# Kernel optimization log

Measured on AMD Instinct MI355X. Metric: run time of the kernel, lower is better.

Reference implementation:

```python
import jax, jax.numpy as jnp
import numpy as np

N = 200000   # 10000 graphs x 20 nodes, stacked
E = 3200000  # avg degree 16
F_IN = 4
H = 32
BN_EPS = 1e-5


def setup_inputs() -> dict:
    key = jax.random.key(0)
    ks = jax.random.split(key, 16)
    s = 0.1
    return {
        "x": jax.random.normal(ks[0], (N, F_IN), jnp.float32),
        "edge_index": jax.random.randint(ks[1], (2, E), 0, N, jnp.int64),
        "edge_weight": jax.random.uniform(ks[2], (E,), jnp.float32),
        "gcn1_w": jax.random.normal(ks[3], (F_IN, H), jnp.float32) * s,
        "gcn1_b": jnp.zeros((H,), jnp.float32),
        "gcn2_w": jax.random.normal(ks[4], (H, H), jnp.float32) * s,
        "gcn2_b": jnp.zeros((H,), jnp.float32),
        "bn1_gamma": jnp.ones((H,), jnp.float32),
        "bn1_beta": jnp.zeros((H,), jnp.float32),
        "bn1_mean": jnp.zeros((H,), jnp.float32),
        "bn1_var": jnp.ones((H,), jnp.float32),
        "bn2_gamma": jnp.ones((H,), jnp.float32),
        "bn2_beta": jnp.zeros((H,), jnp.float32),
        "bn2_mean": jnp.zeros((H,), jnp.float32),
        "bn2_var": jnp.ones((H,), jnp.float32),
        "lstm1_wih": jax.random.normal(ks[5], (4 * H, 2 * H), jnp.float32) * s,
        "lstm1_whh": jax.random.normal(ks[6], (4 * H, H), jnp.float32) * s,
        "lstm1_bih": jax.random.normal(ks[7], (4 * H,), jnp.float32) * s,
        "lstm1_bhh": jax.random.normal(ks[8], (4 * H,), jnp.float32) * s,
        "lstm2_wih": jax.random.normal(ks[9], (4 * H, H), jnp.float32) * s,
        "lstm2_whh": jax.random.normal(ks[10], (4 * H, H), jnp.float32) * s,
        "lstm2_bih": jax.random.normal(ks[11], (4 * H,), jnp.float32) * s,
        "lstm2_bhh": jax.random.normal(ks[12], (4 * H,), jnp.float32) * s,
        "lin_w": jax.random.normal(ks[13], (1, 2 * H + F_IN), jnp.float32) * s,
        "lin_b": jnp.zeros((1,), jnp.float32),
    }


def _gcn_conv(x, src, dst, ew, W, b, n):
    # GCNConv: x @ W, add self-loops (weight 1), symmetric normalization, scatter-add at dst.
    xw = x @ W
    loop = jnp.arange(n)
    s = jnp.concatenate([src, loop])
    d = jnp.concatenate([dst, loop])
    w = jnp.concatenate([ew, jnp.ones((n,), ew.dtype)])
    deg = jax.ops.segment_sum(w, d, num_segments=n)
    dinv = jnp.where(deg > 0, jax.lax.rsqrt(deg), 0.0)
    norm = dinv[s] * w * dinv[d]  # [E+N]
    out = jax.ops.segment_sum(norm[:, None] * xw[s], d, num_segments=n)
    return out + b


def _bn_eval(x, gamma, beta, mean, var):
    return (x - mean) * jax.lax.rsqrt(var + BN_EPS) * gamma + beta


def _lstm_step(x, wih, bih, bhh):
    # single timestep, zero initial (h, c): recurrent W_hh term vanishes.
    gates = x @ wih.T + bih + bhh
    i, f, g, o = jnp.split(gates, 4, axis=1)  # torch gate order i,f,g,o
    c = jax.nn.sigmoid(i) * jnp.tanh(g)
    return jax.nn.sigmoid(o) * jnp.tanh(c)


def reference(x, edge_index, edge_weight, gcn1_w, gcn1_b, gcn2_w, gcn2_b,
              bn1_gamma, bn1_beta, bn1_mean, bn1_var,
              bn2_gamma, bn2_beta, bn2_mean, bn2_var,
              lstm1_wih, lstm1_whh, lstm1_bih, lstm1_bhh,
              lstm2_wih, lstm2_whh, lstm2_bih, lstm2_bhh,
              lin_w, lin_b):
    n = x.shape[0]
    src, dst = edge_index[0], edge_index[1]
    # MPNNLSTM (window=1, eval mode: dropout=identity, BN uses running stats)
    h1 = _bn_eval(jax.nn.relu(_gcn_conv(x, src, dst, edge_weight, gcn1_w, gcn1_b, n)),
                  bn1_gamma, bn1_beta, bn1_mean, bn1_var)
    h2 = _bn_eval(jax.nn.relu(_gcn_conv(h1, src, dst, edge_weight, gcn2_w, gcn2_b, n)),
                  bn2_gamma, bn2_beta, bn2_mean, bn2_var)
    skip = jnp.concatenate([h1, h2], axis=1)  # [N, 2H]
    H1 = _lstm_step(skip, lstm1_wih, lstm1_bih, lstm1_bhh)  # [N, H]
    H2 = _lstm_step(H1, lstm2_wih, lstm2_bih, lstm2_bhh)    # [N, H]
    h = jnp.concatenate([H1, H2, x], axis=1)  # [N, 2H + F_IN]
    # RecurrentGCN head: relu + linear -> [N, 1]
    return jax.nn.relu(h) @ lin_w.T + lin_b
```

## Files before the change

### kernel.cpp

```cpp
#include <hip/hip_runtime.h>
#include <hip/hip_fp16.h>
#include <math.h>

#define BN_EPS 1e-5f
#define HF 32
#define BS 256
#define KEDGE 4096
#define MAXNB 800
#define WQ14 16383.0f
#define WQ22 4194303.0f

typedef _Float16 half8 __attribute__((ext_vector_type(8)));
typedef float f32x4 __attribute__((ext_vector_type(4)));
typedef float f32x2 __attribute__((ext_vector_type(2)));

__device__ __forceinline__ float fsig(float x) {
    return __builtin_amdgcn_rcpf(1.0f + __expf(-x));
}
__device__ __forceinline__ float ftanh(float x) {
    return 1.0f - 2.0f * __builtin_amdgcn_rcpf(1.0f + __expf(2.0f * x));
}


__device__ __forceinline__ float e4m3_to_f32_sw(unsigned v) {
    unsigned s = v & 0x80u, E = (v >> 3) & 0xFu, m = v & 7u;
    float r = E ? ldexpf((float)(8 + m), (int)E - 10) : ldexpf((float)m, -9);
    return s ? -r : r;
}

__device__ __forceinline__ unsigned f32_to_e4m3_sw(float x) {
    float ax = fabsf(x);
    unsigned s = x < 0.0f ? 0x80u : 0u;
    if (!(ax > 0.0f)) return s;
    if (ax >= 448.0f) return s | 0x7Eu;
    int e;
    float m = frexpf(ax, &e);
    int E = e - 1 + 7;
    if (E >= 1) {
        int q = (int)(m * 16.0f + 0.5f);
        if (q == 16) { q = 8; E += 1; if (E > 15) return s | 0x7Eu; }
        return s | (unsigned)(E << 3) | (unsigned)(q - 8);
    }
    int q = (int)(ax * 512.0f + 0.5f);
    if (q > 7) return s | 0x08u;
    return s | (unsigned)q;
}

__device__ __forceinline__ void dec8(uint2 r, float* f) {
#if __has_builtin(__builtin_amdgcn_cvt_pk_f32_fp8)
    f32x2 p0 = __builtin_amdgcn_cvt_pk_f32_fp8((int)r.x, false);
    f32x2 p1 = __builtin_amdgcn_cvt_pk_f32_fp8((int)r.x, true);
    f32x2 p2 = __builtin_amdgcn_cvt_pk_f32_fp8((int)r.y, false);
    f32x2 p3 = __builtin_amdgcn_cvt_pk_f32_fp8((int)r.y, true);
    f[0] = p0[0]; f[1] = p0[1]; f[2] = p1[0]; f[3] = p1[1];
    f[4] = p2[0]; f[5] = p2[1]; f[6] = p3[0]; f[7] = p3[1];
#else
#pragma unroll
    for (int k = 0; k < 4; ++k) f[k] = e4m3_to_f32_sw((r.x >> (8 * k)) & 0xFFu);
#pragma unroll
    for (int k = 0; k < 4; ++k) f[4 + k] = e4m3_to_f32_sw((r.y >> (8 * k)) & 0xFFu);
#endif
}

__device__ __forceinline__ uint2 enc8(const float* o) {
#if __has_builtin(__builtin_amdgcn_cvt_pk_fp8_f32)
    int w0 = 0, w1 = 0;
    w0 = __builtin_amdgcn_cvt_pk_fp8_f32(o[0], o[1], w0, false);
    w0 = __builtin_amdgcn_cvt_pk_fp8_f32(o[2], o[3], w0, true);
    w1 = __builtin_amdgcn_cvt_pk_fp8_f32(o[4], o[5], w1, false);
    w1 = __builtin_amdgcn_cvt_pk_fp8_f32(o[6], o[7], w1, true);
    return make_uint2((unsigned)w0, (unsigned)w1);
#else
    unsigned a = 0, b = 0;
#pragma unroll
    for (int k = 0; k < 4; ++k) a |= f32_to_e4m3_sw(o[k]) << (8 * k);
#pragma unroll
    for (int k = 0; k < 4; ++k) b |= f32_to_e4m3_sw(o[4 + k]) << (8 * k);
    return make_uint2(a, b);
#endif
}


__global__ __launch_bounds__(512) void k_binsort(
        const int* __restrict__ src, const int* __restrict__ dst,
        const float* __restrict__ ew, int E, int NB, int bcap,
        int* __restrict__ gcur, uint2* __restrict__ recs) {
    __shared__ int hist[MAXNB], curs[MAXNB];

    int tid = threadIdx.x;
    int base = blockIdx.x * KEDGE;
    int cnt = min(KEDGE, E - base);

    for (int i = tid; i < NB; i += 512) hist[i] = 0;
    __syncthreads();

    uint2 rec[8];
    int nmine = 0;
    int eb = base + tid * 8;
    if (tid * 8 < cnt) {
        nmine = min(8, cnt - tid * 8);
        if (nmine == 8) {
            int4 s0 = *(const int4*)(src + eb);
            int4 s1 = *(const int4*)(src + eb + 4);
            int4 d0 = *(const int4*)(dst + eb);
            int4 d1 = *(const int4*)(dst + eb + 4);
            float4 w0 = *(const float4*)(ew + eb);
            float4 w1 = *(const float4*)(ew + eb + 4);
            int ss[8] = {s0.x, s0.y, s0.z, s0.w, s1.x, s1.y, s1.z, s1.w};
            int dd[8] = {d0.x, d0.y, d0.z, d0.w, d1.x, d1.y, d1.z, d1.w};
            float ww[8] = {w0.x, w0.y, w0.z, w0.w, w1.x, w1.y, w1.z, w1.w};
#pragma unroll
            for (int k = 0; k < 8; ++k) {
                unsigned q = (unsigned)(ww[k] * WQ22 + 0.5f);
                if (q > 4194303u) q = 4194303u;
                int b = dd[k] >> 8;
                rec[k] = make_uint2(((unsigned)ss[k] << 8) | (unsigned)(dd[k] & 255),
                                    ((unsigned)b << 22) | q);
                atomicAdd(&hist[b], 1);
            }
        } else {
            for (int k = 0; k < nmine; ++k) {
                int s = src[eb + k];
                int d = dst[eb + k];
                float w = ew[eb + k];
                unsigned q = (unsigned)(w * WQ22 + 0.5f);
                if (q > 4194303u) q = 4194303u;
                int b = d >> 8;
                rec[k] = make_uint2(((unsigned)s << 8) | (unsigned)(d & 255),
                                    ((unsigned)b << 22) | q);
                atomicAdd(&hist[b], 1);
            }
        }
    }
    __syncthreads();

    for (int b = tid; b < NB; b += 512) {
        int len = hist[b];
        curs[b] = len ? atomicAdd(&gcur[b], len) : 0;
    }
    __syncthreads();

    for (int k = 0; k < nmine; ++k) {
        uint2 u = rec[k];
        int b = u.y >> 22;
        int off = atomicAdd(&curs[b], 1);
        if (off < bcap) recs[(size_t)b * bcap + off] = u;
    }
}


__global__ __launch_bounds__(512) void k_sortb(
        const uint2* __restrict__ recs, const int* __restrict__ gcur,
        int bcap, int bcap4,
        const float* __restrict__ x, const float* __restrict__ W1,
        unsigned* __restrict__ recs4, int* __restrict__ pstart,
        int* __restrict__ pcnt, float* __restrict__ dinv,
        unsigned char* __restrict__ y18, int n) {
    __shared__ int hist[BS], excl4[BS], curs[BS], wsm[BS];
    __shared__ float sdv[BS];
    __shared__ float sW1[128];

    int b = blockIdx.x, tid = threadIdx.x;
    int cnt = min(gcur[b], bcap);
    const uint2* r = recs + (size_t)b * bcap;
    const float dq = 1.0f / WQ22;

    if (tid < BS) { hist[tid] = 0; wsm[tid] = 0; }
    if (tid >= 256 && tid < 384) sW1[tid - 256] = W1[tid - 256];
    __syncthreads();

    for (int i = tid; i < cnt; i += 512) {
        uint2 u = r[i];
        int dl = u.x & 255;
        atomicAdd(&hist[dl], 1);
        atomicAdd(&wsm[dl], (int)(u.y & 4194303u));
    }
    __syncthreads();

    if (tid < BS) {
        int g = b * BS + tid;
        sdv[tid] = (g < n) ? rsqrtf(1.0f + (float)wsm[tid] * dq) : 0.0f;
    }
    if (tid < 64) {
        int run = 0;
        for (int c = 0; c < BS; c += 64) {
            int idx = c + tid;
            int v = (hist[idx] + 3) & ~3;
            int incl = v;
#pragma unroll
            for (int o = 1; o < 64; o <<= 1) {
                int up = __shfl_up(incl, o, 64);
                if (tid >= o) incl += up;
            }
            int e = run + incl - v;
            excl4[idx] = e; curs[idx] = e;
            run += __shfl(incl, 63, 64);
        }
    }
    __syncthreads();

    unsigned* out4 = recs4 + (size_t)b * bcap4;
    for (int i = tid; i < cnt; i += 512) {
        uint2 u = r[i];
        int dl = u.x & 255;
        int pos = atomicAdd(&curs[dl], 1);
        float qn = (float)(u.y & 4194303u) * dq * sdv[dl];
        unsigned q = (unsigned)(qn * WQ14 + 0.5f);
        if (q > 16383u) q = 16383u;
        out4[pos] = ((u.x >> 8) << 14) | q;
    }

    {
        int node = tid >> 1, half = tid & 1;
        int g = b * BS + node;
        if (g < n) {
            float4 xv = *(const float4*)(x + (size_t)g * 4);
            float sc = sdv[node];
            int f0 = half * 16;
            float o[16];
#pragma unroll
            for (int k = 0; k < 16; ++k)
                o[k] = sc * (xv.x * sW1[f0 + k] + xv.y * sW1[32 + f0 + k] +
                             xv.z * sW1[64 + f0 + k] + xv.w * sW1[96 + f0 + k]);
            uint2 lo = enc8(o), hi = enc8(o + 8);
            *(uint4*)(y18 + ((size_t)g << 5) + half * 16) = make_uint4(lo.x, lo.y, hi.x, hi.y);
        }
    }

    if (tid < BS) {
        int g = b * BS + tid;
        if (g < n) {
            pstart[g] = b * bcap4 + excl4[tid];
            pcnt[g] = hist[tid];
            dinv[g] = sdv[tid];
        }
    }
}


__global__ __launch_bounds__(256) void k_prep(
        const float* __restrict__ wih1, const float* __restrict__ bih1,
        const float* __restrict__ bhh1, const float* __restrict__ wih2,
        const float* __restrict__ bih2, const float* __restrict__ bhh2,
        __half* __restrict__ wp1, __half* __restrict__ wp2,
        float* __restrict__ bsum1, float* __restrict__ bsum2,
        int* __restrict__ gcur, int NB) {
    const int tg[6] = {0, 16, 64, 80, 96, 112};
    int idx = blockIdx.x * 256 + threadIdx.x;
    if (idx < 6144) {
        int t = idx >> 10, rem = idx & 1023;
        int kc = rem >> 9, rem2 = rem & 511;
        int lane = rem2 >> 3, j = rem2 & 7;
        int g = tg[t] + (lane & 15);
        int k = kc * 32 + (lane >> 4) * 8 + j;
        wp1[idx] = __float2half(wih1[g * 64 + k]);
    } else if (idx < 9216) {
        int i2 = idx - 6144;
        int t = i2 >> 9, rem2 = i2 & 511;
        int lane = rem2 >> 3, j = rem2 & 7;
        int g = tg[t] + (lane & 15);
        int k = (lane >> 4) * 8 + j;
        wp2[i2] = __float2half(wih2[g * 32 + k]);
    } else if (idx < 9344) {
        int i = idx - 9216;
        bsum1[i] = bih1[i] + bhh1[i];
    } else if (idx < 9472) {
        int i = idx - 9344;
        bsum2[i] = bih2[i] + bhh2[i];
    } else if (idx < 9472 + NB) {
        gcur[idx - 9472] = 0;
    }
}


__global__ __launch_bounds__(256) void k_g1w2(
        const unsigned* __restrict__ recs4, const int* __restrict__ pstart,
        const int* __restrict__ pcnt, const float* __restrict__ dinv,
        const unsigned char* __restrict__ y18, const float* __restrict__ W2,
        const float* __restrict__ bias, const float* __restrict__ gamma,
        const float* __restrict__ beta, const float* __restrict__ mean,
        const float* __restrict__ var,
        __half* __restrict__ skiph, unsigned char* __restrict__ A8, int n) {
    __shared__ float sW2[1024];
    __shared__ float sh1[64][33];
    int tid = threadIdx.x;
    for (int i = tid; i < 1024; i += 256) sW2[i] = W2[i];
    __syncthreads();

    int nl = tid >> 2;
    int g = blockIdx.x * 64 + nl;
    int lane = tid & 3;
    int fq = lane * 8;
    bool act = g < n;

    float acc[8];
#pragma unroll
    for (int k = 0; k < 8; ++k) acc[k] = 0.0f;

    float dig = 0.0f;
    if (act) {
        dig = dinv[g];
        {
            uint2 sr = ((const uint2*)(y18 + ((size_t)g << 5)))[lane];
            float f[8];
            dec8(sr, f);
#pragma unroll
            for (int k = 0; k < 8; ++k) acc[k] = dig * f[k];
        }

        const float qs = 1.0f / WQ14;
        int cn = pcnt[g];
        const unsigned* r = recs4 + pstart[g];
        uint4 na, nb;
        if (8 <= cn) { na = *(const uint4*)(r); nb = *(const uint4*)(r + 4); }
        int e = 0;
        for (; e + 8 <= cn; e += 8) {
            uint4 ua = na, ub = nb;
            if (e + 16 <= cn) { na = *(const uint4*)(r + e + 8); nb = *(const uint4*)(r + e + 12); }
            unsigned u[8] = {ua.x, ua.y, ua.z, ua.w, ub.x, ub.y, ub.z, ub.w};
            uint2 rw[8];
#pragma unroll
            for (int q = 0; q < 8; ++q)
                rw[q] = ((const uint2*)(y18 + ((size_t)(u[q] >> 14) << 5)))[lane];
            float nm[8];
#pragma unroll
            for (int q = 0; q < 8; ++q)
                nm[q] = (float)(u[q] & 16383u) * qs;
#pragma unroll
            for (int q = 0; q < 8; ++q) {
                float f[8];
                dec8(rw[q], f);
#pragma unroll
                for (int k = 0; k < 8; ++k) acc[k] += nm[q] * f[k];
            }
        }
        for (; e < cn; ++e) {
            unsigned u0 = r[e];
            uint2 r0 = ((const uint2*)(y18 + ((size_t)(u0 >> 14) << 5)))[lane];
            float n0 = (float)(u0 & 16383u) * qs;
            float f[8];
            dec8(r0, f);
#pragma unroll
            for (int k = 0; k < 8; ++k) acc[k] += n0 * f[k];
        }
    }

    float o[8];
#pragma unroll
    for (int k = 0; k < 8; ++k) {
        float v = fmaxf(acc[k] + bias[fq + k], 0.0f);
        o[k] = (v - mean[fq + k]) * gamma[fq + k] * rsqrtf(var[fq + k] + BN_EPS) + beta[fq + k];
        sh1[nl][fq + k] = o[k];
    }
    if (act) {
        union { __half h[8]; uint4 q; } hv;
#pragma unroll
        for (int k = 0; k < 8; ++k) hv.h[k] = __float2half(o[k]);
        *(uint4*)(skiph + (size_t)g * 32 + fq) = hv.q;
    }
    __syncthreads();

    if (act) {
        float a2[8];
#pragma unroll
        for (int j = 0; j < 8; ++j) a2[j] = 0.0f;
#pragma unroll 4
        for (int k = 0; k < 32; ++k) {
            float h = sh1[nl][k];
            const float* wr = sW2 + k * 32 + fq;
#pragma unroll
            for (int j = 0; j < 8; ++j) a2[j] += h * wr[j];
        }
#pragma unroll
        for (int j = 0; j < 8; ++j) a2[j] *= dig;
        ((uint2*)(A8 + ((size_t)g << 5)))[lane] = enc8(a2);
    }
}


__global__ __launch_bounds__(256) void k_g2head(
        const unsigned* __restrict__ recs4, const int* __restrict__ pstart,
        const int* __restrict__ pcnt, const float* __restrict__ dinv,
        const unsigned char* __restrict__ A8,
        const float* __restrict__ bias, const float* __restrict__ gamma,
        const float* __restrict__ beta, const float* __restrict__ mean,
        const float* __restrict__ var,
        const __half* __restrict__ skiph, const float* __restrict__ x,
        const __half* __restrict__ wp1, const __half* __restrict__ wp2,
        const float* __restrict__ bsum1, const float* __restrict__ bsum2,
        const float* __restrict__ lw, const float* __restrict__ lb,
        float* __restrict__ out, int n) {
    __shared__ __align__(16) __half h2s[64][40];
    __shared__ __align__(16) __half H1lds[4 * 16 * 40];
    int tid = threadIdx.x;
    int nl = tid >> 2;
    int g = blockIdx.x * 64 + nl;
    int lane = tid & 3;
    int fq = lane * 8;
    bool act = g < n;

    float acc[8];
#pragma unroll
    for (int k = 0; k < 8; ++k) acc[k] = 0.0f;

    if (act) {
        float dig = dinv[g];
        {
            uint2 sr = ((const uint2*)(A8 + ((size_t)g << 5)))[lane];
            float f[8];
            dec8(sr, f);
#pragma unroll
            for (int k = 0; k < 8; ++k) acc[k] = dig * f[k];
        }

        const float qs = 1.0f / WQ14;
        int cn = pcnt[g];
        const unsigned* r = recs4 + pstart[g];
        uint4 na, nb;
        if (8 <= cn) { na = *(const uint4*)(r); nb = *(const uint4*)(r + 4); }
        int e = 0;
        for (; e + 8 <= cn; e += 8) {
            uint4 ua = na, ub = nb;
            if (e + 16 <= cn) { na = *(const uint4*)(r + e + 8); nb = *(const uint4*)(r + e + 12); }
            unsigned u[8] = {ua.x, ua.y, ua.z, ua.w, ub.x, ub.y, ub.z, ub.w};
            uint2 rw[8];
#pragma unroll
            for (int q = 0; q < 8; ++q)
                rw[q] = ((const uint2*)(A8 + ((size_t)(u[q] >> 14) << 5)))[lane];
            float nm[8];
#pragma unroll
            for (int q = 0; q < 8; ++q)
                nm[q] = (float)(u[q] & 16383u) * qs;
#pragma unroll
            for (int q = 0; q < 8; ++q) {
                float f[8];
                dec8(rw[q], f);
#pragma unroll
                for (int k = 0; k < 8; ++k) acc[k] += nm[q] * f[k];
            }
        }
        for (; e < cn; ++e) {
            unsigned u0 = r[e];
            uint2 r0 = ((const uint2*)(A8 + ((size_t)(u0 >> 14) << 5)))[lane];
            float n0 = (float)(u0 & 16383u) * qs;
            float f0[8];
            dec8(r0, f0);
#pragma unroll
            for (int k = 0; k < 8; ++k) acc[k] += n0 * f0[k];
        }

        union { __half h[8]; uint4 q; } hv;
#pragma unroll
        for (int k = 0; k < 8; ++k) {
            float v = fmaxf(acc[k] + bias[fq + k], 0.0f);
            hv.h[k] = __float2half((v - mean[fq + k]) * gamma[fq + k] *
                                   rsqrtf(var[fq + k] + BN_EPS) + beta[fq + k]);
        }
        *(uint4*)(&h2s[nl][fq]) = hv.q;
    }
    __syncthreads();

    int w = tid >> 6, l = tid & 63;
    int quad = l >> 4, c = l & 15;
    int node_base = blockIdx.x * 64 + w * 16;

    int arow = node_base + c; if (arow > n - 1) arow = n - 1;
    int lr = arow - blockIdx.x * 64;
    half8 a0 = *(const half8*)(skiph + (size_t)arow * 32 + quad * 8);
    half8 a1 = *(const half8*)(&h2s[lr][quad * 8]);

    const half8* b1 = (const half8*)wp1;
    f32x4 d[6];
#pragma unroll
    for (int t = 0; t < 6; ++t) {
        f32x4 ac = {0.0f, 0.0f, 0.0f, 0.0f};
        ac = __builtin_amdgcn_mfma_f32_16x16x32_f16(a0, b1[(t * 2 + 0) * 64 + l], ac, 0, 0, 0);
        ac = __builtin_amdgcn_mfma_f32_16x16x32_f16(a1, b1[(t * 2 + 1) * 64 + l], ac, 0, 0, 0);
        d[t] = ac;
    }

    float bi0 = bsum1[c],      bi1 = bsum1[16 + c];
    float bg0 = bsum1[64 + c], bg1 = bsum1[80 + c];
    float bo0 = bsum1[96 + c], bo1 = bsum1[112 + c];
    float lwc0 = lw[c], lwc1 = lw[c + 16];

    float pa[4];
#pragma unroll
    for (int r = 0; r < 4; ++r) {
        float cc0 = fsig(d[0][r] + bi0) * ftanh(d[2][r] + bg0);
        float h0 = fsig(d[4][r] + bo0) * ftanh(cc0);
        float cc1 = fsig(d[1][r] + bi1) * ftanh(d[3][r] + bg1);
        float h1 = fsig(d[5][r] + bo1) * ftanh(cc1);
        pa[r] = fmaxf(h0, 0.0f) * lwc0 + fmaxf(h1, 0.0f) * lwc1;
        __half* hp = H1lds + (w * 16 + quad * 4 + r) * 40;
        hp[c] = __float2half(h0);
        hp[c + 16] = __float2half(h1);
    }
    __syncthreads();

    half8 a2 = *(const half8*)(H1lds + (w * 16 + c) * 40 + quad * 8);

    const half8* b2 = (const half8*)wp2;
    f32x4 e2[6];
#pragma unroll
    for (int t = 0; t < 6; ++t) {
        f32x4 ac = {0.0f, 0.0f, 0.0f, 0.0f};
        e2[t] = __builtin_amdgcn_mfma_f32_16x16x32_f16(a2, b2[t * 64 + l], ac, 0, 0, 0);
    }

    float ci0 = bsum2[c],      ci1 = bsum2[16 + c];
    float cg0 = bsum2[64 + c], cg1 = bsum2[80 + c];
    float co0 = bsum2[96 + c], co1 = bsum2[112 + c];
    float lw2c0 = lw[32 + c], lw2c1 = lw[48 + c];
#pragma unroll
    for (int r = 0; r < 4; ++r) {
        float cc0 = fsig(e2[0][r] + ci0) * ftanh(e2[2][r] + cg0);
        float h0 = fsig(e2[4][r] + co0) * ftanh(cc0);
        float cc1 = fsig(e2[1][r] + ci1) * ftanh(e2[3][r] + cg1);
        float h1 = fsig(e2[5][r] + co1) * ftanh(cc1);
        pa[r] += fmaxf(h0, 0.0f) * lw2c0 + fmaxf(h1, 0.0f) * lw2c1;
    }

#pragma unroll
    for (int m = 1; m < 16; m <<= 1) {
#pragma unroll
        for (int r = 0; r < 4; ++r) pa[r] += __shfl_xor(pa[r], m, 64);
    }

    if (c < 4) {
        int node = node_base + quad * 4 + c;
        if (node < n) {
            const float4 xv = *(const float4*)(x + (size_t)node * 4);
            out[node] = pa[c] + lb[0]
                + fmaxf(xv.x, 0.0f) * lw[64] + fmaxf(xv.y, 0.0f) * lw[65]
                + fmaxf(xv.z, 0.0f) * lw[66] + fmaxf(xv.w, 0.0f) * lw[67];
        }
    }
}


__global__ void k_initdeg(float* __restrict__ deg, int n) {
    int i = blockIdx.x * blockDim.x + threadIdx.x;
    if (i < n) deg[i] = 1.0f;
}

__global__ void k_deg_only(const int* __restrict__ dst, const float* __restrict__ ew,
                           float* __restrict__ deg, int E) {
    int e = blockIdx.x * blockDim.x + threadIdx.x;
    if (e < E) atomicAdd(&deg[dst[e]], ew[e]);
}

__global__ void k_dinv_f(float* __restrict__ deg, int n) {
    int i = blockIdx.x * blockDim.x + threadIdx.x;
    if (i < n) {
        float d = deg[i];
        deg[i] = d > 0.0f ? rsqrtf(d) : 0.0f;
    }
}

__global__ void k_xw1_f(const float* __restrict__ x, const float* __restrict__ W,
                        float* __restrict__ out, int n) {
    int idx = blockIdx.x * blockDim.x + threadIdx.x;
    if (idx >= n * HF) return;
    int nn = idx >> 5, f = idx & 31;
    const float4 xr = *(const float4*)(x + (size_t)nn * 4);
    out[idx] = xr.x * W[f] + xr.y * W[32 + f] + xr.z * W[64 + f] + xr.w * W[96 + f];
}

__global__ void k_xw2_f(const float* __restrict__ Hin, const float* __restrict__ W,
                        float* __restrict__ out, int n) {
    __shared__ float sW[32 * 32];
    __shared__ float sH[8][32];
    int tid = threadIdx.x;
    for (int i = tid; i < 1024; i += 256) sW[i] = W[i];
    int r = tid >> 5, f = tid & 31;
    int nn = blockIdx.x * 8 + r;
    if (nn < n) sH[r][f] = Hin[(size_t)nn * HF + f];
    __syncthreads();
    if (nn >= n) return;
    float acc = 0.0f;
#pragma unroll
    for (int k = 0; k < 32; ++k) acc += sH[r][k] * sW[k * 32 + f];
    out[(size_t)nn * HF + f] = acc;
}

__global__ void k_selfloop(const float* __restrict__ A, const float* __restrict__ dinv,
                           float* __restrict__ B, int n) {
    int idx = blockIdx.x * blockDim.x + threadIdx.x;
    if (idx >= n * HF) return;
    int nn = idx >> 5;
    float di = dinv[nn];
    B[idx] = di * di * A[idx];
}

__global__ void k_scatter(const int* __restrict__ src, const int* __restrict__ dst,
                          const float* __restrict__ ew, const float* __restrict__ dinv,
                          const float* __restrict__ A, float* __restrict__ B, int total) {
    int idx = blockIdx.x * blockDim.x + threadIdx.x;
    if (idx >= total) return;
    int e = idx >> 5, f = idx & 31;
    int s = src[e], d = dst[e];
    float norm = dinv[s] * ew[e] * dinv[d];
    atomicAdd(&B[d * HF + f], norm * A[s * HF + f]);
}

__global__ void k_post(const float* __restrict__ B, const float* __restrict__ bias,
                       const float* __restrict__ gamma, const float* __restrict__ beta,
                       const float* __restrict__ mean, const float* __restrict__ var,
                       float* __restrict__ Hout, int n) {
    int idx = blockIdx.x * blockDim.x + threadIdx.x;
    if (idx >= n * HF) return;
    int f = idx & 31;
    float v = fmaxf(B[idx] + bias[f], 0.0f);
    float sc = gamma[f] * rsqrtf(var[f] + BN_EPS);
    Hout[idx] = (v - mean[f]) * sc + beta[f];
}

__global__ __launch_bounds__(256) void k_head(
        const float* __restrict__ h1, const float* __restrict__ h2,
        const float* __restrict__ x,
        const float* __restrict__ wih1, const float* __restrict__ bih1, const float* __restrict__ bhh1,
        const float* __restrict__ wih2, const float* __restrict__ bih2, const float* __restrict__ bhh2,
        const float* __restrict__ lw, const float* __restrict__ lb,
        float* __restrict__ out, int n) {
    __shared__ float sH1[32 * 256];
    int tid = threadIdx.x;
    int nn = blockIdx.x * 256 + tid;
    if (nn >= n) return;

    const float4* a = (const float4*)(h1 + (size_t)nn * HF);
    const float4* b = (const float4*)(h2 + (size_t)nn * HF);
    float skip[64];
#pragma unroll
    for (int q = 0; q < 8; ++q) {
        float4 v = a[q];
        skip[4 * q] = v.x; skip[4 * q + 1] = v.y; skip[4 * q + 2] = v.z; skip[4 * q + 3] = v.w;
        float4 u = b[q];
        skip[32 + 4 * q] = u.x; skip[33 + 4 * q] = u.y; skip[34 + 4 * q] = u.z; skip[35 + 4 * q] = u.w;
    }

    float oa = lb[0];
#pragma unroll 1
    for (int j = 0; j < 32; ++j) {
        const float4* wi = (const float4*)(wih1 + (size_t)j * 64);
        const float4* wg = (const float4*)(wih1 + (size_t)(64 + j) * 64);
        const float4* wo = (const float4*)(wih1 + (size_t)(96 + j) * 64);
        float gi = bih1[j] + bhh1[j];
        float gg = bih1[64 + j] + bhh1[64 + j];
        float go = bih1[96 + j] + bhh1[96 + j];
#pragma unroll
        for (int q = 0; q < 16; ++q) {
            float4 aa = wi[q], bb = wg[q], cc4 = wo[q];
            float s0 = skip[4 * q], s1 = skip[4 * q + 1], s2 = skip[4 * q + 2], s3 = skip[4 * q + 3];
            gi += aa.x * s0 + aa.y * s1 + aa.z * s2 + aa.w * s3;
            gg += bb.x * s0 + bb.y * s1 + bb.z * s2 + bb.w * s3;
            go += cc4.x * s0 + cc4.y * s1 + cc4.z * s2 + cc4.w * s3;
        }
        float cc = fsig(gi) * ftanh(gg);
        float hh = fsig(go) * ftanh(cc);
        sH1[j * 256 + tid] = hh;
        oa += fmaxf(hh, 0.0f) * lw[j];
    }

#pragma unroll 1
    for (int j = 0; j < 32; ++j) {
        const float4* wi = (const float4*)(wih2 + (size_t)j * 32);
        const float4* wg = (const float4*)(wih2 + (size_t)(64 + j) * 32);
        const float4* wo = (const float4*)(wih2 + (size_t)(96 + j) * 32);
        float gi = bih2[j] + bhh2[j];
        float gg = bih2[64 + j] + bhh2[64 + j];
        float go = bih2[96 + j] + bhh2[96 + j];
#pragma unroll
        for (int q = 0; q < 8; ++q) {
            float4 aa = wi[q], bb = wg[q], cc4 = wo[q];
            float s0 = sH1[(4 * q) * 256 + tid], s1 = sH1[(4 * q + 1) * 256 + tid];
            float s2 = sH1[(4 * q + 2) * 256 + tid], s3 = sH1[(4 * q + 3) * 256 + tid];
            gi += aa.x * s0 + aa.y * s1 + aa.z * s2 + aa.w * s3;
            gg += bb.x * s0 + bb.y * s1 + bb.z * s2 + bb.w * s3;
            go += cc4.x * s0 + cc4.y * s1 + cc4.z * s2 + cc4.w * s3;
        }
        float cc = fsig(gi) * ftanh(gg);
        float hh = fsig(go) * ftanh(cc);
        oa += fmaxf(hh, 0.0f) * lw[32 + j];
    }

    const float4 xv = *(const float4*)(x + (size_t)nn * 4);
    oa += fmaxf(xv.x, 0.0f) * lw[64] + fmaxf(xv.y, 0.0f) * lw[65] +
          fmaxf(xv.z, 0.0f) * lw[66] + fmaxf(xv.w, 0.0f) * lw[67];
    out[nn] = oa;
}


extern "C" void kernel_launch(void* const* d_in, const int* in_sizes, int n_in,
                              void* d_out, int out_size, void* d_ws, size_t ws_size,
                              hipStream_t stream) {
    const float* x   = (const float*)d_in[0];
    const int*   ei  = (const int*)d_in[1];
    const float* ew  = (const float*)d_in[2];
    const float* g1w = (const float*)d_in[3];
    const float* g1b = (const float*)d_in[4];
    const float* g2w = (const float*)d_in[5];
    const float* g2b = (const float*)d_in[6];
    const float* bn1g = (const float*)d_in[7];
    const float* bn1b = (const float*)d_in[8];
    const float* bn1m = (const float*)d_in[9];
    const float* bn1v = (const float*)d_in[10];
    const float* bn2g = (const float*)d_in[11];
    const float* bn2b = (const float*)d_in[12];
    const float* bn2m = (const float*)d_in[13];
    const float* bn2v = (const float*)d_in[14];
    const float* w1ih = (const float*)d_in[15];
    const float* b1ih = (const float*)d_in[17];
    const float* b1hh = (const float*)d_in[18];
    const float* w2ih = (const float*)d_in[19];
    const float* b2ih = (const float*)d_in[21];
    const float* b2hh = (const float*)d_in[22];
    const float* lw   = (const float*)d_in[23];
    const float* lb   = (const float*)d_in[24];
    float* out = (float*)d_out;

    const int N = in_sizes[0] / 4;
    const int E = in_sizes[2];
    const int* src = ei;
    const int* dst = ei + E;

    const int T = 256;
    const int NB = (N + BS - 1) / BS;
    long long meanb = ((long long)BS * E) / (N > 0 ? N : 1);
    int bcap = (int)(meanb + meanb / 4 + 128);
    bcap = (bcap + 3) & ~3;
    int bcap4 = bcap + 3 * BS;

    char* p = (char*)d_ws;
    auto alloc = [&](size_t bytes) { char* q = p; p += (bytes + 255) & ~(size_t)255; return q; };
    int*      gcur   = (int*)alloc(sizeof(int) * NB);
    uint2*    recs   = (uint2*)alloc(sizeof(uint2) * (size_t)NB * bcap);
    unsigned* recs4  = (unsigned*)alloc(sizeof(unsigned) * (size_t)NB * bcap4);
    float*    dinv   = (float*)alloc(sizeof(float) * N);
    int*      pstart = (int*)alloc(sizeof(int) * N);
    int*      pcnt   = (int*)alloc(sizeof(int) * N);
    unsigned char* y18 = (unsigned char*)alloc((size_t)N * HF);
    unsigned char* A8  = (unsigned char*)alloc((size_t)N * HF);
    __half*   skiph  = (__half*)alloc(sizeof(__half) * (size_t)N * 32);
    __half*   wp1    = (__half*)alloc(sizeof(__half) * 6144);
    __half*   wp2    = (__half*)alloc(sizeof(__half) * 3072);
    float*    bsum1  = (float*)alloc(sizeof(float) * 128);
    float*    bsum2  = (float*)alloc(sizeof(float) * 128);
    size_t need = (size_t)(p - (char*)d_ws);

    int bN  = (N + T - 1) / T;
    int bE  = (E + T - 1) / T;
    int bNF = (N * HF + T - 1) / T;
    int bN8 = (N + 7) / 8;
    int bG  = (N + 63) / 64;
    int bBin = (E + KEDGE - 1) / KEDGE;
    int bPrep = (9472 + NB + 255) / 256;

    if (ws_size >= need && NB <= MAXNB && N <= (1 << 18)) {
        k_prep<<<bPrep, 256, 0, stream>>>(w1ih, b1ih, b1hh, w2ih, b2ih, b2hh,
                                          wp1, wp2, bsum1, bsum2, gcur, NB);
        k_binsort<<<bBin, 512, 0, stream>>>(src, dst, ew, E, NB, bcap, gcur, recs);
        k_sortb<<<NB, 512, 0, stream>>>(recs, gcur, bcap, bcap4, x, g1w,
                                        recs4, pstart, pcnt, dinv, y18, N);

        k_g1w2<<<bG, T, 0, stream>>>(recs4, pstart, pcnt, dinv, y18, g2w,
                                     g1b, bn1g, bn1b, bn1m, bn1v, skiph, A8, N);
        k_g2head<<<bG, T, 0, stream>>>(recs4, pstart, pcnt, dinv, A8,
                                       g2b, bn2g, bn2b, bn2m, bn2v,
                                       skiph, x, wp1, wp2, bsum1, bsum2,
                                       lw, lb, out, N);
    } else {
        size_t Npad = ((size_t)N + 255) & ~(size_t)255;
        float* fdinv = (float*)d_ws;
        float* fA = fdinv + Npad;
        float* fB = fA + (size_t)N * HF;
        float* fC = fB + (size_t)N * HF;
        int bEF = (int)(((long long)E * HF + T - 1) / T);
        int bH = (N + 255) / 256;

        k_initdeg<<<bN, T, 0, stream>>>(fdinv, N);
        k_deg_only<<<bE, T, 0, stream>>>(dst, ew, fdinv, E);
        k_dinv_f<<<bN, T, 0, stream>>>(fdinv, N);

        k_xw1_f<<<bNF, T, 0, stream>>>(x, g1w, fA, N);
        k_selfloop<<<bNF, T, 0, stream>>>(fA, fdinv, fB, N);
        k_scatter<<<bEF, T, 0, stream>>>(src, dst, ew, fdinv, fA, fB, E * HF);
        k_post<<<bNF, T, 0, stream>>>(fB, g1b, bn1g, bn1b, bn1m, bn1v, fC, N);

        k_xw2_f<<<bN8, T, 0, stream>>>(fC, g2w, fA, N);
        k_selfloop<<<bNF, T, 0, stream>>>(fA, fdinv, fB, N);
        k_scatter<<<bEF, T, 0, stream>>>(src, dst, ew, fdinv, fA, fB, E * HF);
        k_post<<<bNF, T, 0, stream>>>(fB, g2b, bn2g, bn2b, bn2m, bn2v, fB, N);

        k_head<<<bH, T, 0, stream>>>(fC, fB, x, w1ih, b1ih, b1hh, w2ih, b2ih, b2hh,
                                     lw, lb, out, N);
    }
}
```

Baseline: 293.7 us.

## Stage bucket records in LDS for sort pass and retune binsort/sortb block sizes

The bucket-sort kernel now caches each bucket's records in shared memory during the histogram pass and reuses them for the scatter pass, so the records are not read from global memory twice. It also moves to 1024 threads with four threads per node for the x@W1 encode. The binning kernel drops to 256 threads and 2048 edges per block, with hist atomics moved after the loads and fully unrolled guarded loops. The large shared array (about 44KB) may limit occupancy, and records past the capacity still fall back to global loads.

```diff
diff --git a/kernel.cpp b/kernel.cpp
--- a/kernel.cpp
+++ b/kernel.cpp
@@ -5,8 +5,9 @@
 #define BN_EPS 1e-5f
 #define HF 32
 #define BS 256
-#define KEDGE 4096
+#define KEDGE 2048
 #define MAXNB 800
+#define SCAP 5504
 #define WQ14 16383.0f
 #define WQ22 4194303.0f
 
@@ -81,7 +82,7 @@
 }
 
 
-__global__ __launch_bounds__(512) void k_binsort(
+__global__ __launch_bounds__(256) void k_binsort(
         const int* __restrict__ src, const int* __restrict__ dst,
         const float* __restrict__ ew, int E, int NB, int bcap,
         int* __restrict__ gcur, uint2* __restrict__ recs) {
@@ -91,35 +92,34 @@
     int base = blockIdx.x * KEDGE;
     int cnt = min(KEDGE, E - base);
 
-    for (int i = tid; i < NB; i += 512) hist[i] = 0;
+    for (int i = tid; i < NB; i += 256) hist[i] = 0;
     __syncthreads();
 
     uint2 rec[8];
-    int nmine = 0;
     int eb = base + tid * 8;
-    if (tid * 8 < cnt) {
-        nmine = min(8, cnt - tid * 8);
-        if (nmine == 8) {
-            int4 s0 = *(const int4*)(src + eb);
-            int4 s1 = *(const int4*)(src + eb + 4);
-            int4 d0 = *(const int4*)(dst + eb);
-            int4 d1 = *(const int4*)(dst + eb + 4);
-            float4 w0 = *(const float4*)(ew + eb);
-            float4 w1 = *(const float4*)(ew + eb + 4);
-            int ss[8] = {s0.x, s0.y, s0.z, s0.w, s1.x, s1.y, s1.z, s1.w};
-            int dd[8] = {d0.x, d0.y, d0.z, d0.w, d1.x, d1.y, d1.z, d1.w};
-            float ww[8] = {w0.x, w0.y, w0.z, w0.w, w1.x, w1.y, w1.z, w1.w};
-#pragma unroll
-            for (int k = 0; k < 8; ++k) {
-                unsigned q = (unsigned)(ww[k] * WQ22 + 0.5f);
-                if (q > 4194303u) q = 4194303u;
-                int b = dd[k] >> 8;
-                rec[k] = make_uint2(((unsigned)ss[k] << 8) | (unsigned)(dd[k] & 255),
-                                    ((unsigned)b << 22) | q);
-                atomicAdd(&hist[b], 1);
-            }
-        } else {
-            for (int k = 0; k < nmine; ++k) {
+    int rem = cnt - tid * 8;
+    if (rem >= 8) {
+        int4 s0 = *(const int4*)(src + eb);
+        int4 s1 = *(const int4*)(src + eb + 4);
+        int4 d0 = *(const int4*)(dst + eb);
+        int4 d1 = *(const int4*)(dst + eb + 4);
+        float4 w0 = *(const float4*)(ew + eb);
+        float4 w1 = *(const float4*)(ew + eb + 4);
+        int ss[8] = {s0.x, s0.y, s0.z, s0.w, s1.x, s1.y, s1.z, s1.w};
+        int dd[8] = {d0.x, d0.y, d0.z, d0.w, d1.x, d1.y, d1.z, d1.w};
+        float ww[8] = {w0.x, w0.y, w0.z, w0.w, w1.x, w1.y, w1.z, w1.w};
+#pragma unroll
+        for (int k = 0; k < 8; ++k) {
+            unsigned q = (unsigned)(ww[k] * WQ22 + 0.5f);
+            if (q > 4194303u) q = 4194303u;
+            int b = dd[k] >> 8;
+            rec[k] = make_uint2(((unsigned)ss[k] << 8) | (unsigned)(dd[k] & 255),
+                                ((unsigned)b << 22) | q);
+        }
+    } else {
+#pragma unroll
+        for (int k = 0; k < 8; ++k) {
+            if (k < rem) {
                 int s = src[eb + k];
                 int d = dst[eb + k];
                 float w = ew[eb + k];
@@ -128,34 +128,40 @@
                 int b = d >> 8;
                 rec[k] = make_uint2(((unsigned)s << 8) | (unsigned)(d & 255),
                                     ((unsigned)b << 22) | q);
-                atomicAdd(&hist[b], 1);
             }
         }
     }
-    __syncthreads();
-
-    for (int b = tid; b < NB; b += 512) {
+#pragma unroll
+    for (int k = 0; k < 8; ++k)
+        if (k < rem) atomicAdd(&hist[rec[k].y >> 22], 1);
+    __syncthreads();
+
+    for (int b = tid; b < NB; b += 256) {
         int len = hist[b];
         curs[b] = len ? atomicAdd(&gcur[b], len) : 0;
     }
     __syncthreads();
 
-    for (int k = 0; k < nmine; ++k) {
-        uint2 u = rec[k];
-        int b = u.y >> 22;
-        int off = atomicAdd(&curs[b], 1);
-        if (off < bcap) recs[(size_t)b * bcap + off] = u;
-    }
-}
-
-
-__global__ __launch_bounds__(512) void k_sortb(
+#pragma unroll
+    for (int k = 0; k < 8; ++k) {
+        if (k < rem) {
+            uint2 u = rec[k];
+            int b = u.y >> 22;
+            int off = atomicAdd(&curs[b], 1);
+            if (off < bcap) recs[(size_t)b * bcap + off] = u;
+        }
+    }
+}
+
+
+__global__ __launch_bounds__(1024) void k_sortb(
         const uint2* __restrict__ recs, const int* __restrict__ gcur,
         int bcap, int bcap4,
         const float* __restrict__ x, const float* __restrict__ W1,
         unsigned* __restrict__ recs4, int* __restrict__ pstart,
         int* __restrict__ pcnt, float* __restrict__ dinv,
         unsigned char* __restrict__ y18, int n) {
+    __shared__ uint2 srec[SCAP];
     __shared__ int hist[BS], excl4[BS], curs[BS], wsm[BS];
     __shared__ float sdv[BS];
     __shared__ float sW1[128];
@@ -169,8 +175,9 @@
     if (tid >= 256 && tid < 384) sW1[tid - 256] = W1[tid - 256];
     __syncthreads();
 
-    for (int i = tid; i < cnt; i += 512) {
+    for (int i = tid; i < cnt; i += 1024) {
         uint2 u = r[i];
+        if (i < SCAP) srec[i] = u;
         int dl = u.x & 255;
         atomicAdd(&hist[dl], 1);
         atomicAdd(&wsm[dl], (int)(u.y & 4194303u));
@@ -200,8 +207,8 @@
     __syncthreads();
 
     unsigned* out4 = recs4 + (size_t)b * bcap4;
-    for (int i = tid; i < cnt; i += 512) {
-        uint2 u = r[i];
+    for (int i = tid; i < cnt; i += 1024) {
+        uint2 u = (i < SCAP) ? srec[i] : r[i];
         int dl = u.x & 255;
         int pos = atomicAdd(&curs[dl], 1);
         float qn = (float)(u.y & 4194303u) * dq * sdv[dl];
@@ -211,19 +218,18 @@
     }
 
     {
-        int node = tid >> 1, half = tid & 1;
+        int node = tid >> 2, q = tid & 3;
         int g = b * BS + node;
         if (g < n) {
             float4 xv = *(const float4*)(x + (size_t)g * 4);
             float sc = sdv[node];
-            int f0 = half * 16;
-            float o[16];
-#pragma unroll
-            for (int k = 0; k < 16; ++k)
+            int f0 = q * 8;
+            float o[8];
+#pragma unroll
+            for (int k = 0; k < 8; ++k)
                 o[k] = sc * (xv.x * sW1[f0 + k] + xv.y * sW1[32 + f0 + k] +
                              xv.z * sW1[64 + f0 + k] + xv.w * sW1[96 + f0 + k]);
-            uint2 lo = enc8(o), hi = enc8(o + 8);
-            *(uint4*)(y18 + ((size_t)g << 5) + half * 16) = make_uint4(lo.x, lo.y, hi.x, hi.y);
+            ((uint2*)(y18 + ((size_t)g << 5)))[q] = enc8(o);
         }
     }
 
@@ -759,9 +765,9 @@
     if (ws_size >= need && NB <= MAXNB && N <= (1 << 18)) {
         k_prep<<<bPrep, 256, 0, stream>>>(w1ih, b1ih, b1hh, w2ih, b2ih, b2hh,
                                           wp1, wp2, bsum1, bsum2, gcur, NB);
-        k_binsort<<<bBin, 512, 0, stream>>>(src, dst, ew, E, NB, bcap, gcur, recs);
-        k_sortb<<<NB, 512, 0, stream>>>(recs, gcur, bcap, bcap4, x, g1w,
-                                        recs4, pstart, pcnt, dinv, y18, N);
+        k_binsort<<<bBin, 256, 0, stream>>>(src, dst, ew, E, NB, bcap, gcur, recs);
+        k_sortb<<<NB, 1024, 0, stream>>>(recs, gcur, bcap, bcap4, x, g1w,
+                                         recs4, pstart, pcnt, dinv, y18, N);
 
         k_g1w2<<<bG, T, 0, stream>>>(recs4, pstart, pcnt, dinv, y18, g2w,
                                      g1b, bn1g, bn1b, bn1m, bn1v, skiph, A8, N);
```

Result: slower. 310.5 us (+5.7%).
